# Performance work log

Measured on AMD Instinct MI355X. Metric: run time of the kernel, lower is better.

Reference implementation:

```python
import jax, jax.numpy as jnp
import numpy as np
import math

B, S, HID, H = 2, 4096, 512, 8
D_K = HID // H


def setup_inputs() -> dict:
    key = jax.random.key(0)
    ks = jax.random.split(key, 8)
    inp = {
        "query": jax.random.normal(ks[0], (B, S, HID), dtype=jnp.float32),
        "key": jax.random.normal(ks[1], (B, S, HID), dtype=jnp.float32),
        "value": jax.random.normal(ks[2], (B, S, HID), dtype=jnp.float32),
        "mask": jax.random.randint(ks[3], (B, S), 0, 2, dtype=jnp.int32),
        # conv1d kernel_size=1, bias=False -> plain [out,in] weights (xavier-normal-ish)
        "Wq": jax.random.normal(ks[4], (HID, HID), dtype=jnp.float32) * (1.0 / math.sqrt(HID)),
        "Wk": jax.random.normal(ks[5], (HID, HID), dtype=jnp.float32) * (1.0 / math.sqrt(HID)),
        "Wv": jax.random.normal(ks[6], (HID, HID), dtype=jnp.float32) * (1.0 / math.sqrt(HID)),
        "Wo": jax.random.normal(ks[7], (HID, HID), dtype=jnp.float32) * (1.0 / math.sqrt(HID)),
    }
    return inp


def reference(query, key, value, mask, Wq, Wk, Wv, Wo):
    b, s, _ = query.shape
    # conv1d(k=1, bias=False) projection == x @ W.T; split heads -> [b,h,s,d_k]
    def proj(x, W):
        return jnp.einsum('bsd,ed->bse', x, W).reshape(b, s, H, D_K).transpose(0, 2, 1, 3)
    q, k, v = proj(query, Wq), proj(key, Wk), proj(value, Wv)
    # NOTE: original scales by 1/log(d_k), not 1/sqrt(d_k)
    score = jnp.einsum('bhqd,bhkd->bhqk', q, k) / math.log(D_K)
    m = mask.reshape(b, 1, 1, s)  # broadcast over heads and query positions
    score = jnp.where(m == 0, jnp.float32(-1e30), score)
    attn = jax.nn.softmax(score, axis=-1)  # dropout is identity in eval
    x = jnp.einsum('bhqk,bhkd->bhqd', attn, v)
    x = x.transpose(0, 2, 1, 3).reshape(b, s, HID)
    return jnp.einsum('bsd,ed->bse', x, Wo)
```

## Files before the change

### kernel.cpp

```cpp
#include <hip/hip_runtime.h>
#include <hip/hip_bf16.h>
#include <cstdint>
#include <cstddef>


namespace {

constexpr int kB = 2, kS = 4096, kHid = 512, kH = 8, kDk = 64;
constexpr int kBH = kB * kH;
constexpr int kM = kB * kS;

typedef __attribute__((ext_vector_type(8))) short short8;
typedef __attribute__((ext_vector_type(2))) float float2v;
typedef __attribute__((ext_vector_type(4))) float floatx4;
typedef __attribute__((ext_vector_type(16))) float floatx16;
typedef __attribute__((ext_vector_type(4))) unsigned int uintx4;
typedef unsigned short u16;

__device__ __forceinline__ u16 bf16rne(float f) {
    uint32_t u = __float_as_uint(f);
    u += 0x7fffu + ((u >> 16) & 1u);
    return (u16)(u >> 16);
}
__device__ __forceinline__ uint32_t pk2(float lo, float hi) {
#if __has_builtin(__builtin_amdgcn_cvt_pk_bf16_f32)
    typedef __attribute__((ext_vector_type(2))) __bf16 bf2;
    bf2 h = __builtin_amdgcn_cvt_pk_bf16_f32(lo, hi);
    return __builtin_bit_cast(uint32_t, h);
#else
    return ((uint32_t)bf16rne(hi) << 16) | (uint32_t)bf16rne(lo);
#endif
}
__device__ __forceinline__ float fexp2(float x) {
#if __has_builtin(__builtin_amdgcn_exp2f)
    return __builtin_amdgcn_exp2f(x);
#else
    return exp2f(x);
#endif
}
__device__ __forceinline__ float bf2f(u16 v) {
    return __uint_as_float((uint32_t)v << 16);
}
__device__ __forceinline__ void plswap(uint32_t& a, uint32_t& b) {
#if __has_builtin(__builtin_amdgcn_permlane32_swap)
    typedef __attribute__((ext_vector_type(2))) unsigned int uint2v;
    uint2v r = __builtin_amdgcn_permlane32_swap(a, b, false, false);
    a = r[0]; b = r[1];
#else
    asm volatile("v_permlane32_swap_b32 %0, %1" : "+v"(a), "+v"(b));
#endif
}
__device__ __forceinline__ void gload16(const void* g, void* l) {
    __builtin_amdgcn_global_load_lds(
        (const __attribute__((address_space(1))) void*)g,
        (__attribute__((address_space(3))) void*)l, 16, 0, 0);
}

__global__ __launch_bounds__(256) void cvt_qw(const float* __restrict__ q,
    const float* __restrict__ k, const float* __restrict__ v,
    const float* __restrict__ w0, const float* __restrict__ w1,
    const float* __restrict__ w2, const float* __restrict__ w3,
    u16* __restrict__ xall, u16* __restrict__ wall) {
    const int bx = blockIdx.x;
    if (bx < 12288) {
        int z = bx >> 12;
        size_t i = (size_t)(bx & 4095) * 256 + threadIdx.x;
        const float* src = z == 0 ? q : (z == 1 ? k : v);
        float4 f = ((const float4*)src)[i];
        ushort4 o;
        o.x = bf16rne(f.x); o.y = bf16rne(f.y);
        o.z = bf16rne(f.z); o.w = bf16rne(f.w);
        ((ushort4*)(xall + (size_t)z * kM * kHid))[i] = o;
    } else {
        int r = bx - 12288;
        int z = r >> 8;
        size_t i = (size_t)(r & 255) * 256 + threadIdx.x;
        const float* src = z == 0 ? w0 : (z == 1 ? w1 : (z == 2 ? w2 : w3));
        float sc = (z == 0)
            ? (float)(1.4426950408889634 / (6.0 * 0.6931471805599453))
            : 1.0f;
        float4 f = ((const float4*)src)[i];
        ushort4 o;
        o.x = bf16rne(f.x * sc); o.y = bf16rne(f.y * sc);
        o.z = bf16rne(f.z * sc); o.w = bf16rne(f.w * sc);
        ((ushort4*)(wall + (size_t)z * kHid * kHid))[i] = o;
    }
}

__global__ __launch_bounds__(256) void cvt_mask(const int* __restrict__ mask,
    float* __restrict__ fb) {
    int i = blockIdx.x * 256 + threadIdx.x;
    fb[i] = mask[i] ? 0.0f : -1e30f;
}

__global__ __launch_bounds__(256, 2) void proj(const u16* __restrict__ xall,
    const u16* __restrict__ wall, u16* __restrict__ qp, u16* __restrict__ kp,
    u16* __restrict__ vt) {
    union PS {
        struct { u16 A[2][128][64]; u16 B[2][128][64]; } s;
        float smt[4][16][68];
    };
    __shared__ __align__(16) PS sm;
    const int z = blockIdx.z;
    const u16* x = xall + (size_t)z * kM * kHid;
    const u16* w = wall + (size_t)z * kHid * kHid;
    const int tid = threadIdx.x;
    const int wv = tid >> 6, lane = tid & 63;
    const int quad = lane >> 4, l16 = lane & 15;
    const int mb = blockIdx.y * 128, nb = blockIdx.x * 128;
    const int mw = (wv >> 1) * 64, nw = (wv & 1) * 64;
    floatx4 acc[4][4] = {};

    const int srow = lane >> 3, sch = lane & 7;
    const int scol = (sch ^ srow) * 8;
    const u16* pA = x + (size_t)(mb + wv * 8 + srow) * kHid + scol;
    const u16* pB = w + (size_t)(nb + wv * 8 + srow) * kHid + scol;
    auto stage = [&](int buf) {
#pragma unroll
        for (int j = 0; j < 4; j++) {
            gload16(pA + (size_t)(j * 32) * kHid, &sm.s.A[buf][j * 32 + wv * 8][0]);
            gload16(pB + (size_t)(j * 32) * kHid, &sm.s.B[buf][j * 32 + wv * 8][0]);
        }
        pA += 64; pB += 64;
    };
    auto compute = [&](int buf) {
#pragma unroll
        for (int hh = 0; hh < 2; hh++) {
            short8 a[4], bt[4];
#pragma unroll
            for (int i = 0; i < 4; i++)
                a[i] = *(const short8*)&sm.s.A[buf][mw + i * 16 + l16]
                        [(((hh << 2) | quad) ^ (l16 & 7)) * 8];
#pragma unroll
            for (int t = 0; t < 4; t++)
                bt[t] = *(const short8*)&sm.s.B[buf][nw + t * 16 + l16]
                        [(((hh << 2) | quad) ^ (l16 & 7)) * 8];
            if (z == 2) {
#pragma unroll
                for (int i = 0; i < 4; i++)
#pragma unroll
                for (int t = 0; t < 4; t++)
                    acc[i][t] = __builtin_amdgcn_mfma_f32_16x16x32_bf16(bt[t], a[i], acc[i][t], 0, 0, 0);
            } else {
#pragma unroll
                for (int i = 0; i < 4; i++)
#pragma unroll
                for (int t = 0; t < 4; t++)
                    acc[i][t] = __builtin_amdgcn_mfma_f32_16x16x32_bf16(a[i], bt[t], acc[i][t], 0, 0, 0);
            }
        }
    };

    stage(0);
    asm volatile("s_waitcnt vmcnt(0)" ::: "memory");
    __builtin_amdgcn_s_barrier();
    int buf = 0;
    for (int t = 0; t < 7; ++t) {
        stage(buf ^ 1);
        compute(buf);
        asm volatile("s_waitcnt vmcnt(0)" ::: "memory");
        __builtin_amdgcn_s_barrier();
        buf ^= 1;
    }
    compute(buf);
    __syncthreads();

    const int mbw = mb + mw, nbw = nb + nw;
    if (z < 2) {
        u16* dst = (z == 0) ? qp : kp;
        const int row16 = lane >> 2, cseg = (lane & 3) * 16;
#pragma unroll
        for (int i = 0; i < 4; i++) {
#pragma unroll
            for (int t = 0; t < 4; t++)
#pragma unroll
            for (int r = 0; r < 4; r++)
                sm.smt[wv][quad * 4 + r][t * 16 + l16] = acc[i][t][r];
            __builtin_amdgcn_wave_barrier();
            const float* rp = &sm.smt[wv][row16][cseg];
            float4 f0 = *(const float4*)(rp);
            float4 f1 = *(const float4*)(rp + 4);
            float4 f2 = *(const float4*)(rp + 8);
            float4 f3 = *(const float4*)(rp + 12);
            uint4 o0, o1;
            o0.x = pk2(f0.x, f0.y); o0.y = pk2(f0.z, f0.w);
            o0.z = pk2(f1.x, f1.y); o0.w = pk2(f1.z, f1.w);
            o1.x = pk2(f2.x, f2.y); o1.y = pk2(f2.z, f2.w);
            o1.z = pk2(f3.x, f3.y); o1.w = pk2(f3.z, f3.w);
            u16* dp = dst + (size_t)(mbw + i * 16 + row16) * kHid + nbw + cseg;
            *(uint4*)dp = o0;
            *(uint4*)(dp + 8) = o1;
            __builtin_amdgcn_wave_barrier();
        }
    } else {
        const int b = mbw >> 12, s0 = mbw & (kS - 1);
        const int row16 = lane >> 2, cseg = (lane & 3) * 16;
#pragma unroll
        for (int t = 0; t < 4; t++) {
#pragma unroll
            for (int i = 0; i < 4; i++)
#pragma unroll
            for (int r = 0; r < 4; r++)
                sm.smt[wv][quad * 4 + r][i * 16 + l16] = acc[i][t][r];
            __builtin_amdgcn_wave_barrier();
            const float* rp = &sm.smt[wv][row16][cseg];
            float4 f0 = *(const float4*)(rp);
            float4 f1 = *(const float4*)(rp + 4);
            float4 f2 = *(const float4*)(rp + 8);
            float4 f3 = *(const float4*)(rp + 12);
            uint4 o0, o1;
            o0.x = pk2(f0.x, f0.y); o0.y = pk2(f0.z, f0.w);
            o0.z = pk2(f1.x, f1.y); o0.w = pk2(f1.z, f1.w);
            o1.x = pk2(f2.x, f2.y); o1.y = pk2(f2.z, f2.w);
            o1.z = pk2(f3.x, f3.y); o1.w = pk2(f3.z, f3.w);
            const int n = nbw + t * 16 + row16;
            const int h = n >> 6, d = n & (kDk - 1);
            u16* dp = vt + ((size_t)(b * kH + h) * kDk + d) * kS + s0 + cseg;
            *(uint4*)dp = o0;
            *(uint4*)(dp + 8) = o1;
            __builtin_amdgcn_wave_barrier();
        }
    }
}

__global__ __launch_bounds__(256, 2) void attn(const u16* __restrict__ qp,
    const u16* __restrict__ kp, const u16* __restrict__ vt,
    const float* __restrict__ fbias, u16* __restrict__ ows,
    float* __restrict__ rsws) {
    union SmT {
        struct { u16 K[3][64][64]; u16 V[3][64][64]; float B[3][256]; } s;
        float ep[4][32][33];
    };
    __shared__ __align__(16) SmT sm;
    const int tid = threadIdx.x;
    const int wv = tid >> 6, l = tid & 63;
    const int hf = l >> 5, q32 = l & 31, l7 = l & 7;
    const int wg = blockIdx.x;
    const int bh = ((wg & 7) << 1) | ((wg >> 3) & 1);
    const int qb = (wg >> 4) & 15;
    const int kz = wg >> 8;
    const int b = bh >> 3, h = bh & 7;
    const int qbase = qb * 256 + wv * 64;
    const u16* Qb = qp + (size_t)b * kS * kHid + h * 64;
    const u16* Kb = kp + (size_t)b * kS * kHid + h * 64;
    const u16* Vb = vt + (size_t)bh * kDk * kS;
    const float* fm = fbias + b * kS;

    short8 qf[2][4];
#pragma unroll
    for (int qt = 0; qt < 2; qt++)
#pragma unroll
    for (int m = 0; m < 4; m++)
        qf[qt][m] = *(const short8*)(Qb + (size_t)(qbase + qt * 32 + q32) * kHid + m * 16 + hf * 8);

    floatx16 O[2][2] = {};
    float rs[2] = {0.0f, 0.0f};

    const int srow = l >> 3;
    const int pcol = (l7 ^ srow) * 8;
    const u16* pK = Kb + (size_t)(kz * 64 + wv * 8 + srow) * kHid + pcol;
    const u16* pV = Vb + (size_t)(wv * 8 + srow) * kS + kz * 64 + pcol;
    const float* pB = fm + kz * 64 + (l & 15) * 4;
    auto stage = [&](int buf) {
        gload16(pK,                     &sm.s.K[buf][wv * 8][0]);
        gload16(pK + (size_t)32 * kHid, &sm.s.K[buf][wv * 8 + 32][0]);
        gload16(pV,                     &sm.s.V[buf][wv * 8][0]);
        gload16(pV + (size_t)32 * kS,   &sm.s.V[buf][wv * 8 + 32][0]);
        gload16(pB,                     &sm.s.B[buf][0]);
        pK += (size_t)128 * kHid;
        pV += 128;
        pB += 128;
    };

    auto compute = [&](int buf) {
#pragma unroll
        for (int ks = 0; ks < 2; ++ks) {
            short8 kf[4];
#pragma unroll
            for (int m = 0; m < 4; m++)
                kf[m] = *(const short8*)&sm.s.K[buf][ks * 32 + q32][((2 * m + hf) ^ l7) * 8];
            short8 vf[2][2];
#pragma unroll
            for (int ds = 0; ds < 2; ds++)
#pragma unroll
            for (int tt = 0; tt < 2; tt++)
                vf[ds][tt] = *(const short8*)&sm.s.V[buf][ds * 32 + q32][((ks * 4 + tt * 2 + hf) ^ l7) * 8];
            const float* bb = &sm.s.B[buf][ks * 32 + 4 * hf];
            float4 g0 = *(const float4*)(bb);
            float4 g1 = *(const float4*)(bb + 8);
            float4 g2 = *(const float4*)(bb + 16);
            float4 g3 = *(const float4*)(bb + 24);
#pragma unroll
            for (int qt = 0; qt < 2; ++qt) {
                floatx16 st;
                st[0] = g0.x;  st[1] = g0.y;  st[2] = g0.z;  st[3] = g0.w;
                st[4] = g1.x;  st[5] = g1.y;  st[6] = g1.z;  st[7] = g1.w;
                st[8] = g2.x;  st[9] = g2.y;  st[10] = g2.z; st[11] = g2.w;
                st[12] = g3.x; st[13] = g3.y; st[14] = g3.z; st[15] = g3.w;
#pragma unroll
                for (int m = 0; m < 4; m++)
                    st = __builtin_amdgcn_mfma_f32_32x32x16_bf16(kf[m], qf[qt][m], st, 0, 0, 0);
                float xx[16];
#pragma unroll
                for (int r = 0; r < 16; r++) xx[r] = fexp2(st[r]);
                float2v a0 = {xx[0], xx[1]},  a1 = {xx[2], xx[3]};
                float2v a2 = {xx[4], xx[5]},  a3 = {xx[6], xx[7]};
                float2v a4 = {xx[8], xx[9]},  a5 = {xx[10], xx[11]};
                float2v a6 = {xx[12], xx[13]}, a7 = {xx[14], xx[15]};
                a0 += a1; a2 += a3; a4 += a5; a6 += a7;
                a0 += a2; a4 += a6;
                a0 += a4;
                rs[qt] += a0[0] + a0[1];
                uint32_t w00 = pk2(xx[0], xx[1]),   w01 = pk2(xx[2], xx[3]);
                uint32_t w10 = pk2(xx[4], xx[5]),   w11 = pk2(xx[6], xx[7]);
                uint32_t w20 = pk2(xx[8], xx[9]),   w21 = pk2(xx[10], xx[11]);
                uint32_t w30 = pk2(xx[12], xx[13]), w31 = pk2(xx[14], xx[15]);
                plswap(w00, w10); plswap(w01, w11);
                plswap(w20, w30); plswap(w21, w31);
                uintx4 t0 = {w00, w01, w10, w11};
                uintx4 t1 = {w20, w21, w30, w31};
                short8 bf0 = __builtin_bit_cast(short8, t0);
                short8 bf1 = __builtin_bit_cast(short8, t1);
                O[qt][0] = __builtin_amdgcn_mfma_f32_32x32x16_bf16(vf[0][0], bf0, O[qt][0], 0, 0, 0);
                O[qt][0] = __builtin_amdgcn_mfma_f32_32x32x16_bf16(vf[0][1], bf1, O[qt][0], 0, 0, 0);
                O[qt][1] = __builtin_amdgcn_mfma_f32_32x32x16_bf16(vf[1][0], bf0, O[qt][1], 0, 0, 0);
                O[qt][1] = __builtin_amdgcn_mfma_f32_32x32x16_bf16(vf[1][1], bf1, O[qt][1], 0, 0, 0);
            }
        }
    };

    stage(0);
    stage(1);
    for (int t = 0; t < 30; ++t) {
        asm volatile("s_waitcnt vmcnt(5)" ::: "memory");
        __builtin_amdgcn_s_barrier();
        __builtin_amdgcn_sched_barrier(0);
        stage((t + 2) % 3);
        compute(t % 3);
    }
    asm volatile("s_waitcnt vmcnt(5)" ::: "memory");
    __builtin_amdgcn_s_barrier();
    __builtin_amdgcn_sched_barrier(0);
    compute(0);
    asm volatile("s_waitcnt vmcnt(0)" ::: "memory");
    __builtin_amdgcn_s_barrier();
    __builtin_amdgcn_sched_barrier(0);
    compute(1);
    __syncthreads();

#pragma unroll
    for (int qt = 0; qt < 2; ++qt) {
        float r = rs[qt];
        r += __shfl_xor(r, 32);
        if (hf == 0)
            rsws[((size_t)kz * kBH + bh) * kS + qbase + qt * 32 + q32] = r;
        u16* Ob = ows + (((size_t)kz * kBH + bh) * kS + qbase + qt * 32) * kDk;
#pragma unroll
        for (int ds = 0; ds < 2; ds++) {
#pragma unroll
            for (int rr = 0; rr < 16; rr++)
                sm.ep[wv][q32][(rr & 3) + 8 * (rr >> 2) + 4 * hf] = O[qt][ds][rr];
            __builtin_amdgcn_wave_barrier();
            {
                const int qq = l >> 1, c0 = (l & 1) * 16;
                float f[16];
#pragma unroll
                for (int j = 0; j < 16; j++) f[j] = sm.ep[wv][qq][c0 + j];
                uint4 o0, o1;
                o0.x = pk2(f[0], f[1]);   o0.y = pk2(f[2], f[3]);
                o0.z = pk2(f[4], f[5]);   o0.w = pk2(f[6], f[7]);
                o1.x = pk2(f[8], f[9]);   o1.y = pk2(f[10], f[11]);
                o1.z = pk2(f[12], f[13]); o1.w = pk2(f[14], f[15]);
                u16* dp = Ob + (size_t)qq * kDk + ds * 32 + c0;
                *(uint4*)dp = o0;
                *(uint4*)(dp + 8) = o1;
            }
            __builtin_amdgcn_wave_barrier();
        }
    }
}

__global__ __launch_bounds__(256) void combine(const u16* __restrict__ ows,
    const float* __restrict__ rsws, u16* __restrict__ xo) {
    size_t i = (size_t)blockIdx.x * 256 + threadIdx.x;
    const int d8 = (int)(i & 7);
    const int s  = (int)((i >> 3) & (kS - 1));
    const int bh = (int)(i >> 15);
    const int b = bh >> 3, h = bh & 7;
    const size_t base = ((size_t)bh * kS + s) * kDk + d8 * 8;
    short8 a = *(const short8*)(ows + base);
    short8 c = *(const short8*)(ows + (size_t)kBH * kS * kDk + base);
    float r = rsws[(size_t)bh * kS + s] + rsws[(size_t)kBH * kS + (size_t)bh * kS + s];
    float inv = 1.0f / r;
    float e[8];
#pragma unroll
    for (int j = 0; j < 8; j++)
        e[j] = (bf2f((u16)a[j]) + bf2f((u16)c[j])) * inv;
    uint4 o;
    o.x = pk2(e[0], e[1]); o.y = pk2(e[2], e[3]);
    o.z = pk2(e[4], e[5]); o.w = pk2(e[6], e[7]);
    *(uint4*)(xo + ((size_t)b * kS + s) * kHid + h * 64 + d8 * 8) = o;
}

__global__ __launch_bounds__(256, 2) void oproj(const u16* __restrict__ x,
    const u16* __restrict__ w, float* __restrict__ out) {
    __shared__ __align__(16) u16 A[2][128][64];
    __shared__ __align__(16) u16 Bt[2][128][64];
    const int tid = threadIdx.x;
    const int wv = tid >> 6, lane = tid & 63;
    const int quad = lane >> 4, l16 = lane & 15;
    const int mb = blockIdx.y * 128, nb = blockIdx.x * 128;
    const int mw = (wv >> 1) * 64, nw = (wv & 1) * 64;
    floatx4 acc[4][4] = {};
    const int srow = lane >> 3, sch = lane & 7;
    const int scol = (sch ^ srow) * 8;
    const u16* pA = x + (size_t)(mb + wv * 8 + srow) * kHid + scol;
    const u16* pB = w + (size_t)(nb + wv * 8 + srow) * kHid + scol;
    auto stage = [&](int buf) {
#pragma unroll
        for (int j = 0; j < 4; j++) {
            gload16(pA + (size_t)(j * 32) * kHid, &A[buf][j * 32 + wv * 8][0]);
            gload16(pB + (size_t)(j * 32) * kHid, &Bt[buf][j * 32 + wv * 8][0]);
        }
        pA += 64; pB += 64;
    };
    auto compute = [&](int buf) {
#pragma unroll
        for (int hh = 0; hh < 2; hh++) {
            short8 a[4], bt[4];
#pragma unroll
            for (int i = 0; i < 4; i++)
                a[i] = *(const short8*)&A[buf][mw + i * 16 + l16]
                        [(((hh << 2) | quad) ^ (l16 & 7)) * 8];
#pragma unroll
            for (int t = 0; t < 4; t++)
                bt[t] = *(const short8*)&Bt[buf][nw + t * 16 + l16]
                        [(((hh << 2) | quad) ^ (l16 & 7)) * 8];
#pragma unroll
            for (int i = 0; i < 4; i++)
#pragma unroll
            for (int t = 0; t < 4; t++)
                acc[i][t] = __builtin_amdgcn_mfma_f32_16x16x32_bf16(a[i], bt[t], acc[i][t], 0, 0, 0);
        }
    };

    stage(0);
    asm volatile("s_waitcnt vmcnt(0)" ::: "memory");
    __builtin_amdgcn_s_barrier();
    int buf = 0;
    for (int t = 0; t < 7; ++t) {
        stage(buf ^ 1);
        compute(buf);
        asm volatile("s_waitcnt vmcnt(0)" ::: "memory");
        __builtin_amdgcn_s_barrier();
        buf ^= 1;
    }
    compute(buf);

    const int mbw = mb + mw, nbw = nb + nw;
#pragma unroll
    for (int i = 0; i < 4; i++)
#pragma unroll
    for (int t = 0; t < 4; t++)
#pragma unroll
    for (int r = 0; r < 4; r++) {
        int m = mbw + i * 16 + quad * 4 + r;
        int n = nbw + t * 16 + l16;
        out[(size_t)m * kHid + n] = acc[i][t][r];
    }
}

}

extern "C" void kernel_launch(void* const* d_in, const int* in_sizes, int n_in,
                              void* d_out, int out_size, void* d_ws, size_t ws_size,
                              hipStream_t stream) {
    const float* q  = (const float*)d_in[0];
    const float* k  = (const float*)d_in[1];
    const float* v  = (const float*)d_in[2];
    const int* mask = (const int*)d_in[3];
    const float* w0 = (const float*)d_in[4];
    const float* w1 = (const float*)d_in[5];
    const float* w2 = (const float*)d_in[6];
    const float* w3 = (const float*)d_in[7];
    float* out = (float*)d_out;

    u16* ws   = (u16*)d_ws;
    u16* xall = ws;
    u16* wall = xall + (size_t)3 * kM * kHid;
    u16* qp   = wall + (size_t)4 * kHid * kHid;
    u16* kp   = qp + (size_t)kBH * kS * kDk;
    u16* vt   = kp + (size_t)kBH * kS * kDk;
    u16* ows  = xall;
    float* fbias = (float*)wall;
    float* rsws  = fbias + (size_t)kB * kS;
    u16* xo   = qp;

    dim3 blk(256);
    cvt_qw <<<dim3(13312), blk, 0, stream>>>(q, k, v, w0, w1, w2, w3, xall, wall);
    proj   <<<dim3(kHid / 128, kM / 128, 3), blk, 0, stream>>>(xall, wall, qp, kp, vt);
    cvt_mask<<<dim3(kB * kS / 256), blk, 0, stream>>>(mask, fbias);
    attn   <<<dim3(512), blk, 0, stream>>>(qp, kp, vt, fbias, ows, rsws);
    combine<<<dim3(2048), blk, 0, stream>>>(ows, rsws, xo);
    oproj  <<<dim3(kHid / 128, kM / 128), blk, 0, stream>>>(
        xo, wall + (size_t)3 * kHid * kHid, out);
}
```

Measured before the change: 234.0 us.

## Fuse fp32-to-bf16 activation conversion into projection GEMM A-tile loading

The separate pass that converted query/key/value activations to bf16 is removed. The projection kernel now loads fp32 activations into registers, packs them to bf16 and writes them into swizzled LDS, while B tiles still use direct global-to-LDS loads. This drops a full write and re-read of the bf16 activation buffers and one large kernel launch. In exchange the GEMM reads twice as many activation bytes, uses more registers, and waits for the register loads before the LDS write each iteration, which reduces overlap.

```diff
diff --git a/kernel.cpp b/kernel.cpp
--- a/kernel.cpp
+++ b/kernel.cpp
@@ -56,35 +56,21 @@
         (__attribute__((address_space(3))) void*)l, 16, 0, 0);
 }
 
-__global__ __launch_bounds__(256) void cvt_qw(const float* __restrict__ q,
-    const float* __restrict__ k, const float* __restrict__ v,
-    const float* __restrict__ w0, const float* __restrict__ w1,
-    const float* __restrict__ w2, const float* __restrict__ w3,
-    u16* __restrict__ xall, u16* __restrict__ wall) {
+__global__ __launch_bounds__(256) void cvt_w(const float* __restrict__ w0,
+    const float* __restrict__ w1, const float* __restrict__ w2,
+    const float* __restrict__ w3, u16* __restrict__ wall) {
     const int bx = blockIdx.x;
-    if (bx < 12288) {
-        int z = bx >> 12;
-        size_t i = (size_t)(bx & 4095) * 256 + threadIdx.x;
-        const float* src = z == 0 ? q : (z == 1 ? k : v);
-        float4 f = ((const float4*)src)[i];
-        ushort4 o;
-        o.x = bf16rne(f.x); o.y = bf16rne(f.y);
-        o.z = bf16rne(f.z); o.w = bf16rne(f.w);
-        ((ushort4*)(xall + (size_t)z * kM * kHid))[i] = o;
-    } else {
-        int r = bx - 12288;
-        int z = r >> 8;
-        size_t i = (size_t)(r & 255) * 256 + threadIdx.x;
-        const float* src = z == 0 ? w0 : (z == 1 ? w1 : (z == 2 ? w2 : w3));
-        float sc = (z == 0)
-            ? (float)(1.4426950408889634 / (6.0 * 0.6931471805599453))
-            : 1.0f;
-        float4 f = ((const float4*)src)[i];
-        ushort4 o;
-        o.x = bf16rne(f.x * sc); o.y = bf16rne(f.y * sc);
-        o.z = bf16rne(f.z * sc); o.w = bf16rne(f.w * sc);
-        ((ushort4*)(wall + (size_t)z * kHid * kHid))[i] = o;
-    }
+    const int z = bx >> 8;
+    size_t i = (size_t)(bx & 255) * 256 + threadIdx.x;
+    const float* src = z == 0 ? w0 : (z == 1 ? w1 : (z == 2 ? w2 : w3));
+    float sc = (z == 0)
+        ? (float)(1.4426950408889634 / (6.0 * 0.6931471805599453))
+        : 1.0f;
+    float4 f = ((const float4*)src)[i];
+    ushort4 o;
+    o.x = bf16rne(f.x * sc); o.y = bf16rne(f.y * sc);
+    o.z = bf16rne(f.z * sc); o.w = bf16rne(f.w * sc);
+    ((ushort4*)(wall + (size_t)z * kHid * kHid))[i] = o;
 }
 
 __global__ __launch_bounds__(256) void cvt_mask(const int* __restrict__ mask,
@@ -93,7 +79,8 @@
     fb[i] = mask[i] ? 0.0f : -1e30f;
 }
 
-__global__ __launch_bounds__(256, 2) void proj(const u16* __restrict__ xall,
+__global__ __launch_bounds__(256, 2) void proj(const float* __restrict__ xq,
+    const float* __restrict__ xk, const float* __restrict__ xv,
     const u16* __restrict__ wall, u16* __restrict__ qp, u16* __restrict__ kp,
     u16* __restrict__ vt) {
     union PS {
@@ -102,7 +89,7 @@
     };
     __shared__ __align__(16) PS sm;
     const int z = blockIdx.z;
-    const u16* x = xall + (size_t)z * kM * kHid;
+    const float* x = z == 0 ? xq : (z == 1 ? xk : xv);
     const u16* w = wall + (size_t)z * kHid * kHid;
     const int tid = threadIdx.x;
     const int wv = tid >> 6, lane = tid & 63;
@@ -111,17 +98,35 @@
     const int mw = (wv >> 1) * 64, nw = (wv & 1) * 64;
     floatx4 acc[4][4] = {};
 
+    const int arow = tid >> 1, ahalf = tid & 1;
+    const float* pAsrc = x + (size_t)(mb + arow) * kHid + ahalf * 32;
     const int srow = lane >> 3, sch = lane & 7;
     const int scol = (sch ^ srow) * 8;
-    const u16* pA = x + (size_t)(mb + wv * 8 + srow) * kHid + scol;
     const u16* pB = w + (size_t)(nb + wv * 8 + srow) * kHid + scol;
-    auto stage = [&](int buf) {
+
+    float4 areg[8];
+    auto loadA = [&]() {
+#pragma unroll
+        for (int j = 0; j < 8; j++)
+            areg[j] = *(const float4*)(pAsrc + j * 4);
+        pAsrc += 64;
+    };
+    auto stageB = [&](int buf) {
+#pragma unroll
+        for (int j = 0; j < 4; j++)
+            gload16(pB + (size_t)(j * 32) * kHid, &sm.s.B[buf][j * 32 + wv * 8][0]);
+        pB += 64;
+    };
+    auto writeA = [&](int buf) {
 #pragma unroll
         for (int j = 0; j < 4; j++) {
-            gload16(pA + (size_t)(j * 32) * kHid, &sm.s.A[buf][j * 32 + wv * 8][0]);
-            gload16(pB + (size_t)(j * 32) * kHid, &sm.s.B[buf][j * 32 + wv * 8][0]);
-        }
-        pA += 64; pB += 64;
+            uintx4 u = {pk2(areg[2 * j].x, areg[2 * j].y),
+                        pk2(areg[2 * j].z, areg[2 * j].w),
+                        pk2(areg[2 * j + 1].x, areg[2 * j + 1].y),
+                        pk2(areg[2 * j + 1].z, areg[2 * j + 1].w)};
+            const int c = ahalf * 4 + j;
+            *(uintx4*)&sm.s.A[buf][arow][(c ^ (arow & 7)) * 8] = u;
+        }
     };
     auto compute = [&](int buf) {
 #pragma unroll
@@ -151,15 +156,18 @@
         }
     };
 
-    stage(0);
+    loadA(); stageB(0);
     asm volatile("s_waitcnt vmcnt(0)" ::: "memory");
-    __builtin_amdgcn_s_barrier();
+    writeA(0);
+    __syncthreads();
     int buf = 0;
     for (int t = 0; t < 7; ++t) {
-        stage(buf ^ 1);
+        loadA();
+        stageB(buf ^ 1);
         compute(buf);
         asm volatile("s_waitcnt vmcnt(0)" ::: "memory");
-        __builtin_amdgcn_s_barrier();
+        writeA(buf ^ 1);
+        __syncthreads();
         buf ^= 1;
     }
     compute(buf);
@@ -486,19 +494,19 @@
     float* out = (float*)d_out;
 
     u16* ws   = (u16*)d_ws;
-    u16* xall = ws;
-    u16* wall = xall + (size_t)3 * kM * kHid;
+    u16* owsreg = ws;
+    u16* wall = owsreg + (size_t)3 * kM * kHid;
     u16* qp   = wall + (size_t)4 * kHid * kHid;
     u16* kp   = qp + (size_t)kBH * kS * kDk;
     u16* vt   = kp + (size_t)kBH * kS * kDk;
-    u16* ows  = xall;
+    u16* ows  = owsreg;
     float* fbias = (float*)wall;
     float* rsws  = fbias + (size_t)kB * kS;
     u16* xo   = qp;
 
     dim3 blk(256);
-    cvt_qw <<<dim3(13312), blk, 0, stream>>>(q, k, v, w0, w1, w2, w3, xall, wall);
-    proj   <<<dim3(kHid / 128, kM / 128, 3), blk, 0, stream>>>(xall, wall, qp, kp, vt);
+    cvt_w  <<<dim3(1024), blk, 0, stream>>>(w0, w1, w2, w3, wall);
+    proj   <<<dim3(kHid / 128, kM / 128, 3), blk, 0, stream>>>(q, k, v, wall, qp, kp, vt);
     cvt_mask<<<dim3(kB * kS / 256), blk, 0, stream>>>(mask, fbias);
     attn   <<<dim3(512), blk, 0, stream>>>(qp, kp, vt, fbias, ows, rsws);
     combine<<<dim3(2048), blk, 0, stream>>>(ows, rsws, xo);
```

New measurement: 243.3 us. 1.04x slower.

## Triple-buffer projection GEMMs with K=32 stages and fold mask conversion into cvt kernel

Applied to the files above, without the earlier changes.

The proj and oproj GEMMs move from double-buffered K=64 tiles to triple-buffered K=32 tiles, with partial vmcnt waits so global-to-LDS loads overlap compute across two stages in flight. proj raises its occupancy hint to 3 blocks per CU and swaps grid axes. oproj halves its M tile to 64 to launch more blocks. The mask-to-bias conversion is merged into the conversion kernel, saving one launch, and the bias is stored in the output buffer as scratch before oproj overwrites it. The cost is more barriers per K step and a tighter register budget.

```diff
diff --git a/kernel.cpp b/kernel.cpp
--- a/kernel.cpp
+++ b/kernel.cpp
@@ -60,7 +60,8 @@
     const float* __restrict__ k, const float* __restrict__ v,
     const float* __restrict__ w0, const float* __restrict__ w1,
     const float* __restrict__ w2, const float* __restrict__ w3,
-    u16* __restrict__ xall, u16* __restrict__ wall) {
+    const int* __restrict__ mask,
+    u16* __restrict__ xall, u16* __restrict__ wall, float* __restrict__ fb) {
     const int bx = blockIdx.x;
     if (bx < 12288) {
         int z = bx >> 12;
@@ -71,7 +72,7 @@
         o.x = bf16rne(f.x); o.y = bf16rne(f.y);
         o.z = bf16rne(f.z); o.w = bf16rne(f.w);
         ((ushort4*)(xall + (size_t)z * kM * kHid))[i] = o;
-    } else {
+    } else if (bx < 13312) {
         int r = bx - 12288;
         int z = r >> 8;
         size_t i = (size_t)(r & 255) * 256 + threadIdx.x;
@@ -84,20 +85,17 @@
         o.x = bf16rne(f.x * sc); o.y = bf16rne(f.y * sc);
         o.z = bf16rne(f.z * sc); o.w = bf16rne(f.w * sc);
         ((ushort4*)(wall + (size_t)z * kHid * kHid))[i] = o;
-    }
-}
-
-__global__ __launch_bounds__(256) void cvt_mask(const int* __restrict__ mask,
-    float* __restrict__ fb) {
-    int i = blockIdx.x * 256 + threadIdx.x;
-    fb[i] = mask[i] ? 0.0f : -1e30f;
-}
-
-__global__ __launch_bounds__(256, 2) void proj(const u16* __restrict__ xall,
+    } else {
+        int i = (bx - 13312) * 256 + threadIdx.x;
+        fb[i] = mask[i] ? 0.0f : -1e30f;
+    }
+}
+
+__global__ __launch_bounds__(256, 3) void proj(const u16* __restrict__ xall,
     const u16* __restrict__ wall, u16* __restrict__ qp, u16* __restrict__ kp,
     u16* __restrict__ vt) {
     union PS {
-        struct { u16 A[2][128][64]; u16 B[2][128][64]; } s;
+        struct { u16 A[3][128][32]; u16 B[3][128][32]; } s;
         float smt[4][16][68];
     };
     __shared__ __align__(16) PS sm;
@@ -107,62 +105,63 @@
     const int tid = threadIdx.x;
     const int wv = tid >> 6, lane = tid & 63;
     const int quad = lane >> 4, l16 = lane & 15;
-    const int mb = blockIdx.y * 128, nb = blockIdx.x * 128;
+    const int mb = blockIdx.x * 128, nb = blockIdx.y * 128;
     const int mw = (wv >> 1) * 64, nw = (wv & 1) * 64;
     floatx4 acc[4][4] = {};
 
-    const int srow = lane >> 3, sch = lane & 7;
-    const int scol = (sch ^ srow) * 8;
-    const u16* pA = x + (size_t)(mb + wv * 8 + srow) * kHid + scol;
-    const u16* pB = w + (size_t)(nb + wv * 8 + srow) * kHid + scol;
+    const int srow = lane >> 2;
+    const int scol = ((lane & 3) ^ (srow & 3)) * 8;
+    const u16* pA = x + (size_t)(mb + wv * 16 + srow) * kHid + scol;
+    const u16* pB = w + (size_t)(nb + wv * 16 + srow) * kHid + scol;
     auto stage = [&](int buf) {
-#pragma unroll
-        for (int j = 0; j < 4; j++) {
-            gload16(pA + (size_t)(j * 32) * kHid, &sm.s.A[buf][j * 32 + wv * 8][0]);
-            gload16(pB + (size_t)(j * 32) * kHid, &sm.s.B[buf][j * 32 + wv * 8][0]);
+        gload16(pA,                     &sm.s.A[buf][wv * 16][0]);
+        gload16(pA + (size_t)64 * kHid, &sm.s.A[buf][64 + wv * 16][0]);
+        gload16(pB,                     &sm.s.B[buf][wv * 16][0]);
+        gload16(pB + (size_t)64 * kHid, &sm.s.B[buf][64 + wv * 16][0]);
+        pA += 32; pB += 32;
+    };
+    auto compute = [&](int buf) {
+        short8 a[4], bt[4];
+#pragma unroll
+        for (int i = 0; i < 4; i++)
+            a[i] = *(const short8*)&sm.s.A[buf][mw + i * 16 + l16]
+                    [(quad ^ (l16 & 3)) * 8];
+#pragma unroll
+        for (int t = 0; t < 4; t++)
+            bt[t] = *(const short8*)&sm.s.B[buf][nw + t * 16 + l16]
+                    [(quad ^ (l16 & 3)) * 8];
+        if (z == 2) {
+#pragma unroll
+            for (int i = 0; i < 4; i++)
+#pragma unroll
+            for (int t = 0; t < 4; t++)
+                acc[i][t] = __builtin_amdgcn_mfma_f32_16x16x32_bf16(bt[t], a[i], acc[i][t], 0, 0, 0);
+        } else {
+#pragma unroll
+            for (int i = 0; i < 4; i++)
+#pragma unroll
+            for (int t = 0; t < 4; t++)
+                acc[i][t] = __builtin_amdgcn_mfma_f32_16x16x32_bf16(a[i], bt[t], acc[i][t], 0, 0, 0);
         }
-        pA += 64; pB += 64;
-    };
-    auto compute = [&](int buf) {
-#pragma unroll
-        for (int hh = 0; hh < 2; hh++) {
-            short8 a[4], bt[4];
-#pragma unroll
-            for (int i = 0; i < 4; i++)
-                a[i] = *(const short8*)&sm.s.A[buf][mw + i * 16 + l16]
-                        [(((hh << 2) | quad) ^ (l16 & 7)) * 8];
-#pragma unroll
-            for (int t = 0; t < 4; t++)
-                bt[t] = *(const short8*)&sm.s.B[buf][nw + t * 16 + l16]
-                        [(((hh << 2) | quad) ^ (l16 & 7)) * 8];
-            if (z == 2) {
-#pragma unroll
-                for (int i = 0; i < 4; i++)
-#pragma unroll
-                for (int t = 0; t < 4; t++)
-                    acc[i][t] = __builtin_amdgcn_mfma_f32_16x16x32_bf16(bt[t], a[i], acc[i][t], 0, 0, 0);
-            } else {
-#pragma unroll
-                for (int i = 0; i < 4; i++)
-#pragma unroll
-                for (int t = 0; t < 4; t++)
-                    acc[i][t] = __builtin_amdgcn_mfma_f32_16x16x32_bf16(a[i], bt[t], acc[i][t], 0, 0, 0);
-            }
-        }
     };
 
     stage(0);
+    stage(1);
+    for (int t = 0; t < 14; ++t) {
+        asm volatile("s_waitcnt vmcnt(4)" ::: "memory");
+        __builtin_amdgcn_s_barrier();
+        __builtin_amdgcn_sched_barrier(0);
+        stage((t + 2) % 3);
+        compute(t % 3);
+    }
+    asm volatile("s_waitcnt vmcnt(4)" ::: "memory");
+    __builtin_amdgcn_s_barrier();
+    __builtin_amdgcn_sched_barrier(0);
+    compute(2);
     asm volatile("s_waitcnt vmcnt(0)" ::: "memory");
     __builtin_amdgcn_s_barrier();
-    int buf = 0;
-    for (int t = 0; t < 7; ++t) {
-        stage(buf ^ 1);
-        compute(buf);
-        asm volatile("s_waitcnt vmcnt(0)" ::: "memory");
-        __builtin_amdgcn_s_barrier();
-        buf ^= 1;
-    }
-    compute(buf);
+    __builtin_amdgcn_sched_barrier(0);
+    compute(0);
     __syncthreads();
 
     const int mbw = mb + mw, nbw = nb + nw;
@@ -404,62 +403,60 @@
 
 __global__ __launch_bounds__(256, 2) void oproj(const u16* __restrict__ x,
     const u16* __restrict__ w, float* __restrict__ out) {
-    __shared__ __align__(16) u16 A[2][128][64];
-    __shared__ __align__(16) u16 Bt[2][128][64];
+    __shared__ __align__(16) u16 A[3][64][32];
+    __shared__ __align__(16) u16 Bt[3][128][32];
     const int tid = threadIdx.x;
     const int wv = tid >> 6, lane = tid & 63;
     const int quad = lane >> 4, l16 = lane & 15;
-    const int mb = blockIdx.y * 128, nb = blockIdx.x * 128;
-    const int mw = (wv >> 1) * 64, nw = (wv & 1) * 64;
-    floatx4 acc[4][4] = {};
-    const int srow = lane >> 3, sch = lane & 7;
-    const int scol = (sch ^ srow) * 8;
-    const u16* pA = x + (size_t)(mb + wv * 8 + srow) * kHid + scol;
-    const u16* pB = w + (size_t)(nb + wv * 8 + srow) * kHid + scol;
+    const int mb = blockIdx.x * 64, nb = blockIdx.y * 128;
+    const int mw = (wv >> 1) * 32, nw = (wv & 1) * 64;
+    floatx4 acc[2][4] = {};
+    const int srow = lane >> 2;
+    const int scol = ((lane & 3) ^ (srow & 3)) * 8;
+    const u16* pA = x + (size_t)(mb + wv * 16 + srow) * kHid + scol;
+    const u16* pB = w + (size_t)(nb + wv * 16 + srow) * kHid + scol;
     auto stage = [&](int buf) {
-#pragma unroll
-        for (int j = 0; j < 4; j++) {
-            gload16(pA + (size_t)(j * 32) * kHid, &A[buf][j * 32 + wv * 8][0]);
-            gload16(pB + (size_t)(j * 32) * kHid, &Bt[buf][j * 32 + wv * 8][0]);
-        }
-        pA += 64; pB += 64;
+        gload16(pA,                     &A[buf][wv * 16][0]);
+        gload16(pB,                     &Bt[buf][wv * 16][0]);
+        gload16(pB + (size_t)64 * kHid, &Bt[buf][64 + wv * 16][0]);
+        pA += 32; pB += 32;
     };
     auto compute = [&](int buf) {
-#pragma unroll
-        for (int hh = 0; hh < 2; hh++) {
-            short8 a[4], bt[4];
-#pragma unroll
-            for (int i = 0; i < 4; i++)
-                a[i] = *(const short8*)&A[buf][mw + i * 16 + l16]
-                        [(((hh << 2) | quad) ^ (l16 & 7)) * 8];
-#pragma unroll
-            for (int t = 0; t < 4; t++)
-                bt[t] = *(const short8*)&Bt[buf][nw + t * 16 + l16]
-                        [(((hh << 2) | quad) ^ (l16 & 7)) * 8];
-#pragma unroll
-            for (int i = 0; i < 4; i++)
-#pragma unroll
-            for (int t = 0; t < 4; t++)
-                acc[i][t] = __builtin_amdgcn_mfma_f32_16x16x32_bf16(a[i], bt[t], acc[i][t], 0, 0, 0);
-        }
+        short8 a[2], bt[4];
+#pragma unroll
+        for (int i = 0; i < 2; i++)
+            a[i] = *(const short8*)&A[buf][mw + i * 16 + l16][(quad ^ (l16 & 3)) * 8];
+#pragma unroll
+        for (int t = 0; t < 4; t++)
+            bt[t] = *(const short8*)&Bt[buf][nw + t * 16 + l16][(quad ^ (l16 & 3)) * 8];
+#pragma unroll
+        for (int i = 0; i < 2; i++)
+#pragma unroll
+        for (int t = 0; t < 4; t++)
+            acc[i][t] = __builtin_amdgcn_mfma_f32_16x16x32_bf16(a[i], bt[t], acc[i][t], 0, 0, 0);
     };
 
     stage(0);
+    stage(1);
+    for (int t = 0; t < 14; ++t) {
+        asm volatile("s_waitcnt vmcnt(3)" ::: "memory");
+        __builtin_amdgcn_s_barrier();
+        __builtin_amdgcn_sched_barrier(0);
+        stage((t + 2) % 3);
+        compute(t % 3);
+    }
+    asm volatile("s_waitcnt vmcnt(3)" ::: "memory");
+    __builtin_amdgcn_s_barrier();
+    __builtin_amdgcn_sched_barrier(0);
+    compute(2);
     asm volatile("s_waitcnt vmcnt(0)" ::: "memory");
     __builtin_amdgcn_s_barrier();
-    int buf = 0;
-    for (int t = 0; t < 7; ++t) {
-        stage(buf ^ 1);
-        compute(buf);
-        asm volatile("s_waitcnt vmcnt(0)" ::: "memory");
-        __builtin_amdgcn_s_barrier();
-        buf ^= 1;
-    }
-    compute(buf);
+    __builtin_amdgcn_sched_barrier(0);
+    compute(0);
 
     const int mbw = mb + mw, nbw = nb + nw;
 #pragma unroll
-    for (int i = 0; i < 4; i++)
+    for (int i = 0; i < 2; i++)
 #pragma unroll
     for (int t = 0; t < 4; t++)
 #pragma unroll
@@ -492,16 +489,16 @@
     u16* kp   = qp + (size_t)kBH * kS * kDk;
     u16* vt   = kp + (size_t)kBH * kS * kDk;
     u16* ows  = xall;
-    float* fbias = (float*)wall;
-    float* rsws  = fbias + (size_t)kB * kS;
+    float* rsws  = (float*)wall;
+    float* fbias = out;
     u16* xo   = qp;
 
     dim3 blk(256);
-    cvt_qw <<<dim3(13312), blk, 0, stream>>>(q, k, v, w0, w1, w2, w3, xall, wall);
-    proj   <<<dim3(kHid / 128, kM / 128, 3), blk, 0, stream>>>(xall, wall, qp, kp, vt);
-    cvt_mask<<<dim3(kB * kS / 256), blk, 0, stream>>>(mask, fbias);
+    cvt_qw <<<dim3(13344), blk, 0, stream>>>(q, k, v, w0, w1, w2, w3, mask,
+                                             xall, wall, fbias);
+    proj   <<<dim3(kM / 128, kHid / 128, 3), blk, 0, stream>>>(xall, wall, qp, kp, vt);
     attn   <<<dim3(512), blk, 0, stream>>>(qp, kp, vt, fbias, ows, rsws);
     combine<<<dim3(2048), blk, 0, stream>>>(ows, rsws, xo);
-    oproj  <<<dim3(kHid / 128, kM / 128), blk, 0, stream>>>(
+    oproj  <<<dim3(kM / 64, kHid / 128), blk, 0, stream>>>(
         xo, wall + (size_t)3 * kHid * kHid, out);
 }
```

Measured after the change: 225.5 us. -3.6%, faster.
